# Kernel optimization log

Hardware: AMD Instinct MI355X
Metric: run time of the kernel (lower is better)

The kernel has to match this reference:

```python
import jax, jax.numpy as jnp
import numpy as np

GRID_SIZE = 8
MARGIN = 1.0
NUM_NEG = 4
SOS_NEG = 8
LOSS_LAMBDA = 1.0
IMG_H, IMG_W = 960, 1280  # desc2 is the stride-GRID_SIZE feature map of this image
BIG = 5.0    # fill for radius-masked entries in FOS distance matrix (> max unit-desc dist 2)
HUGE = 1e6   # fill for invalid entries in SOS candidate scores


def _l2n(x, eps=1e-8):
    return x / (jnp.linalg.norm(x, axis=-1, keepdims=True) + eps)


def _pdist(a, b, eps=1e-12):
    # a: B x N x C, b: B x M x C -> B x N x M euclidean distances
    sq = (jnp.sum(a * a, -1)[..., :, None] + jnp.sum(b * b, -1)[..., None, :]
          - 2.0 * jnp.einsum('bnc,bmc->bnm', a, b))
    return jnp.sqrt(jnp.maximum(sq, eps))


def _bilinear(desc, pts):
    # desc: B x C x H x W, pts: B x N x 2 in (y, x) image-pixel coords -> B x N x C
    B, C, H, W = desc.shape
    g = pts / GRID_SIZE - 0.5  # image coords -> feature-grid coords
    gy = jnp.clip(g[..., 0], 0.0, H - 1.0)
    gx = jnp.clip(g[..., 1], 0.0, W - 1.0)
    y0 = jnp.clip(jnp.floor(gy).astype(jnp.int32), 0, H - 2)
    x0 = jnp.clip(jnp.floor(gx).astype(jnp.int32), 0, W - 2)
    wy = (gy - y0)[:, None, :]
    wx = (gx - x0)[:, None, :]
    flat = desc.reshape(B, C, H * W)
    gat = lambda yi, xi: jnp.take_along_axis(flat, (yi * W + xi)[:, None, :], axis=2)
    v00, v01 = gat(y0, x0), gat(y0, x0 + 1)
    v10, v11 = gat(y0 + 1, x0), gat(y0 + 1, x0 + 1)
    out = (v00 * (1 - wy) * (1 - wx) + v01 * (1 - wy) * wx
           + v10 * wy * (1 - wx) + v11 * wy * wx)
    return out.transpose(0, 2, 1)


def _forward(kp1, w_kp1, kp1_desc, desc2, homo12):
    r = 2.0 * GRID_SIZE  # spatial masking radius
    d1 = _l2n(kp1_desc)                       # B x N x C
    w_desc = _l2n(_bilinear(desc2, w_kp1))    # B x N x C interpolated warped descriptors

    # visibility of kp1 under homography homo12 (kp stored as (y, x))
    ones = jnp.ones_like(kp1[..., :1])
    p = jnp.concatenate([kp1[..., 1:2], kp1[..., 0:1], ones], -1)  # (x, y, 1)
    q = jnp.einsum('bij,bnj->bni', homo12, p)
    qx = q[..., 0] / (q[..., 2] + 1e-8)
    qy = q[..., 1] / (q[..., 2] + 1e-8)
    vis = ((qx >= 0) & (qx < IMG_W) & (qy >= 0) & (qy < IMG_H)).astype(d1.dtype)
    denom = jnp.sum(vis) + 1e-8

    # ---- FOS: hard quad triplet with radius masking ----
    pos = jnp.sqrt(jnp.sum((d1 - w_desc) ** 2, -1) + 1e-12)  # B x N
    D = _pdist(d1, w_desc)          # B x N x N cross descriptor distances
    s22 = _pdist(w_kp1, w_kp1)      # B x N x N warped-coordinate distances
    Dm = jnp.where(s22 <= r, BIG, D)  # mask spatial near-positives (incl. diagonal)
    neg1 = -jax.lax.top_k(-Dm, NUM_NEG)[0]                       # hardest negs per row anchor
    neg2 = -jax.lax.top_k(-Dm.transpose(0, 2, 1), NUM_NEG)[0]    # per column anchor
    t1 = jnp.mean(jax.nn.relu(MARGIN + pos[..., None] - neg1), -1)
    t2 = jnp.mean(jax.nn.relu(MARGIN + pos[..., None] - neg2), -1)
    fos = jnp.sum(vis * 0.5 * (t1 + t2)) / denom

    # ---- SOS: radius-masked second-order similarity regularizer ----
    s11 = _pdist(kp1, kp1)
    d11 = _pdist(d1, d1)
    d22 = _pdist(w_desc, w_desc)
    valid = (s11 > r) & (s22 > r)
    score = jnp.where(valid, d11, HUGE)
    nscore, idx = jax.lax.top_k(-score, SOS_NEG)  # sos_neg hardest valid neighbors
    sel_d11 = -nscore
    sel_d22 = jnp.take_along_axis(d22, idx, axis=2)
    diff2 = jnp.where(sel_d11 < HUGE * 0.1, (sel_d11 - sel_d22) ** 2, 0.0)
    sos_i = jnp.sqrt(jnp.sum(diff2, -1) + 1e-12)
    sos = jnp.sum(vis * sos_i) / denom

    return (fos + sos) * LOSS_LAMBDA


def setup_inputs() -> dict:
    key = jax.random.key(0)
    k1, k2, k3, k4, k5 = jax.random.split(key, 5)
    B, N, C, H, W = 2, 4096, 128, 120, 160
    scale = jnp.array([IMG_H - 1.0, IMG_W - 1.0], dtype=jnp.float32)
    kp1 = jax.random.uniform(k1, (B, N, 2), dtype=jnp.float32) * scale
    w_kp1 = jax.random.uniform(k2, (B, N, 2), dtype=jnp.float32) * scale
    kp1_desc = jax.random.normal(k3, (B, N, C), dtype=jnp.float32)
    desc2 = jax.random.normal(k4, (B, C, H, W), dtype=jnp.float32)
    homo12 = (jnp.tile(jnp.eye(3, dtype=jnp.float32), (B, 1, 1))
              + 0.001 * jax.random.normal(k5, (B, 3, 3), dtype=jnp.float32))
    return {'kp1': kp1, 'w_kp1': w_kp1, 'kp1_desc': kp1_desc,
            'desc2': desc2, 'homo12': homo12}


def reference(kp1, w_kp1, kp1_desc, desc2, homo12):
    return _forward(kp1, w_kp1, kp1_desc, desc2, homo12)
```

## Files before the change

kernel.cpp:

```cpp
#include <hip/hip_runtime.h>
#include <hip/hip_fp16.h>
#include <math.h>

#define NPTS 4096
#define CDIM 128
#define FH 120
#define FW 160
#define PIX (FH * FW)

typedef __attribute__((ext_vector_type(8))) short short8_t;
typedef __attribute__((ext_vector_type(4))) float float4_t;
typedef __attribute__((ext_vector_type(2))) unsigned short ushort2_t;

#define OFF_FRAG  0
#define OFF_WDB   1048576
#define OFF_JA    1572864
#define OFF_JB    1605632
#define OFF_POS   1622016
#define OFF_VIS   1630208
#define OFF_ACC   1638400
#define OFF_D2T   2031632
#define OFF_PARTS 2031632
#define OFF_END   4489232

__device__ __forceinline__ unsigned short f2bf(float f) {
  unsigned int u = __float_as_uint(f);
  u = (u + 0x7fffu + ((u >> 16) & 1u)) >> 16;
  return (unsigned short)u;
}

__device__ __forceinline__ float wavesum(float v) {
#pragma unroll
  for (int off = 1; off < 64; off <<= 1) v += __shfl_xor(v, off, 64);
  return v;
}

typedef const __attribute__((address_space(1))) unsigned int gu32_t;
typedef __attribute__((address_space(3))) unsigned int lu32_t;
__device__ __forceinline__ void gl_lds16(const void* g, void* l) {
  __builtin_amdgcn_global_load_lds((gu32_t*)g, (lu32_t*)l, 16, 0, 0);
}

__global__ __launch_bounds__(256) void transpose_desc2(
    const float* __restrict__ d2, unsigned short* __restrict__ out) {
  __shared__ unsigned short tile[64][130];
  const int bp = blockIdx.x;
  const int b = bp / 300;
  const int p0 = (bp - b * 300) * 64;
  const int tid = threadIdx.x;
  const int grp = tid >> 6, lp = tid & 63;
#pragma unroll 4
  for (int r = 0; r < 32; ++r) {
    int c = (r << 2) | grp;
    float v = d2[((size_t)b * CDIM + c) * PIX + p0 + lp];
    tile[lp][c] = __half_as_ushort(__float2half(v));
  }
  __syncthreads();
  unsigned int* ob = (unsigned int*)(out + ((size_t)b * PIX + p0) * CDIM);
#pragma unroll
  for (int i = 0; i < 16; ++i) {
    int u = (i << 8) | tid;
    int p = u >> 6, cc = (u & 63) << 1;
    unsigned int lo = tile[p][cc], hi = tile[p][cc + 1];
    ob[u] = lo | (hi << 16);
  }
}

#define PREP_TAIL() do {                                                        \
  {                                                                             \
    const int T = (p & (NPTS - 1)) >> 4, cRow = p & 15;                         \
    const int kcL = lane >> 4, quadL = (lane >> 2) & 3, jjL = (lane & 3) * 2;   \
    const size_t off = (size_t)(quadL * 16 + cRow) * 8 + jjL;                   \
    const size_t tb = (((size_t)b * 256 + T) * 2) * 4;                          \
    ushort2_t st; st.x = f2bf(d0); st.y = f2bf(d1v);                            \
    ushort2_t sw; sw.x = f2bf(e0); sw.y = f2bf(e1);                             \
    *(ushort2_t*)(frag + (tb + kcL) * 512 + off) = st;                          \
    *(ushort2_t*)(frag + (tb + 4 + kcL) * 512 + off) = sw;                      \
    ushort2_t swr; swr.x = f2bf(e0); swr.y = f2bf(e1);                          \
    *(ushort2_t*)(wdb + (size_t)p * CDIM + c2) = swr;                           \
  }                                                                             \
  float dd0 = d0 - e0, dd1 = d1v - e1;                                          \
  float ssp = wavesum(dd0 * dd0 + dd1 * dd1);                                   \
  if (lane == 0) {                                                              \
    pos[p] = sqrtf(ssp + 1e-12f);                                               \
    float ky = kp1[p * 2 + 0], kx = kp1[p * 2 + 1];                             \
    jA[p] = make_float4(ky, kx, y, x);                                          \
    jB[p] = make_float2(n1, n2);                                                \
    const float* h = homo + b * 9;                                              \
    float t0 = h[0] * kx + h[1] * ky + h[2];                                    \
    float t1 = h[3] * kx + h[4] * ky + h[5];                                    \
    float t2 = h[6] * kx + h[7] * ky + h[8];                                    \
    float qx = t0 / (t2 + 1e-8f), qy = t1 / (t2 + 1e-8f);                       \
    vis[p] = (qx >= 0.0f && qx < 1280.0f && qy >= 0.0f && qy < 960.0f)          \
                 ? 1.0f : 0.0f;                                                 \
  }                                                                             \
} while (0)

__global__ __launch_bounds__(256) void prep_t(
    const float* __restrict__ kp1, const float* __restrict__ wkp1,
    const float* __restrict__ desc, const unsigned short* __restrict__ d2t,
    const float* __restrict__ homo,
    unsigned short* __restrict__ frag, unsigned short* __restrict__ wdb,
    float4* __restrict__ jA, float2* __restrict__ jB,
    float* __restrict__ pos, float* __restrict__ vis, float* __restrict__ acc) {
  const int tid = threadIdx.x;
  if (blockIdx.x == 0 && tid < 4) acc[tid] = 0.0f;
  const int p = blockIdx.x * 4 + (tid >> 6);
  const int lane = tid & 63;
  const int b = p >> 12;
  const int c2 = lane * 2;

  float2 v = *(const float2*)(desc + (size_t)p * CDIM + c2);
  float ss = wavesum(v.x * v.x + v.y * v.y);
  float inv = 1.0f / (sqrtf(ss) + 1e-8f);
  float d0 = v.x * inv, d1v = v.y * inv;
  float n1 = ss * inv * inv;

  float y = wkp1[p * 2 + 0], x = wkp1[p * 2 + 1];
  float gy = fminf(fmaxf(y * 0.125f - 0.5f, 0.0f), (float)(FH - 1));
  float gx = fminf(fmaxf(x * 0.125f - 0.5f, 0.0f), (float)(FW - 1));
  int y0 = (int)floorf(gy); y0 = min(max(y0, 0), FH - 2);
  int x0 = (int)floorf(gx); x0 = min(max(x0, 0), FW - 2);
  float wy = gy - (float)y0, wx = gx - (float)x0;
  float w00 = (1 - wy) * (1 - wx), w01 = (1 - wy) * wx;
  float w10 = wy * (1 - wx), w11 = wy * wx;
  const unsigned int* t00 = (const unsigned int*)
      (d2t + ((size_t)b * PIX + y0 * FW + x0) * CDIM) + lane;
  unsigned int u00 = t00[0], u01 = t00[64];
  unsigned int u10 = t00[FW * 64], u11 = t00[FW * 64 + 64];
  float2 f00 = __half22float2(*(const __half2*)&u00);
  float2 f01 = __half22float2(*(const __half2*)&u01);
  float2 f10 = __half22float2(*(const __half2*)&u10);
  float2 f11 = __half22float2(*(const __half2*)&u11);
  float wv0 = f00.x * w00 + f01.x * w01 + f10.x * w10 + f11.x * w11;
  float wv1 = f00.y * w00 + f01.y * w01 + f10.y * w10 + f11.y * w11;
  float ss2 = wavesum(wv0 * wv0 + wv1 * wv1);
  float inv2 = 1.0f / (sqrtf(ss2) + 1e-8f);
  float e0 = wv0 * inv2, e1 = wv1 * inv2;
  float n2 = ss2 * inv2 * inv2;

  PREP_TAIL();
}

__global__ __launch_bounds__(256) void prep_g(
    const float* __restrict__ kp1, const float* __restrict__ wkp1,
    const float* __restrict__ desc, const float* __restrict__ desc2,
    const float* __restrict__ homo,
    unsigned short* __restrict__ frag, unsigned short* __restrict__ wdb,
    float4* __restrict__ jA, float2* __restrict__ jB,
    float* __restrict__ pos, float* __restrict__ vis, float* __restrict__ acc) {
  const int tid = threadIdx.x;
  if (blockIdx.x == 0 && tid < 4) acc[tid] = 0.0f;
  const int p = blockIdx.x * 4 + (tid >> 6);
  const int lane = tid & 63;
  const int b = p >> 12;
  const int c2 = lane * 2;

  float2 v = *(const float2*)(desc + (size_t)p * CDIM + c2);
  float ss = wavesum(v.x * v.x + v.y * v.y);
  float inv = 1.0f / (sqrtf(ss) + 1e-8f);
  float d0 = v.x * inv, d1v = v.y * inv;
  float n1 = ss * inv * inv;

  float y = wkp1[p * 2 + 0], x = wkp1[p * 2 + 1];
  float gy = fminf(fmaxf(y * 0.125f - 0.5f, 0.0f), (float)(FH - 1));
  float gx = fminf(fmaxf(x * 0.125f - 0.5f, 0.0f), (float)(FW - 1));
  int y0 = (int)floorf(gy); y0 = min(max(y0, 0), FH - 2);
  int x0 = (int)floorf(gx); x0 = min(max(x0, 0), FW - 2);
  float wy = gy - (float)y0, wx = gx - (float)x0;
  float w00 = (1 - wy) * (1 - wx), w01 = (1 - wy) * wx;
  float w10 = wy * (1 - wx), w11 = wy * wx;
  const float* q0 = desc2 + ((size_t)b * CDIM + c2) * PIX + y0 * FW + x0;
  const float* q1 = q0 + PIX;
  float wv0 = q0[0] * w00 + q0[1] * w01 + q0[FW] * w10 + q0[FW + 1] * w11;
  float wv1 = q1[0] * w00 + q1[1] * w01 + q1[FW] * w10 + q1[FW + 1] * w11;
  float ss2 = wavesum(wv0 * wv0 + wv1 * wv1);
  float inv2 = 1.0f / (sqrtf(ss2) + 1e-8f);
  float e0 = wv0 * inv2, e1 = wv1 * inv2;
  float n2 = ss2 * inv2 * inv2;

  PREP_TAIL();
}

__device__ __forceinline__ void ins4m(float v, float* L) {
  float p0 = L[0]; L[0] = fmaxf(L[0], v);
  float p1 = L[1]; L[1] = __builtin_amdgcn_fmed3f(p0, L[1], v);
  float p2 = L[2]; L[2] = __builtin_amdgcn_fmed3f(p1, L[2], v);
  L[3] = __builtin_amdgcn_fmed3f(p2, L[3], v);
}
__device__ __forceinline__ void ins6m(float v, float* L) {
  float p0 = L[0]; L[0] = fmaxf(L[0], v);
  float p1 = L[1]; L[1] = __builtin_amdgcn_fmed3f(p0, L[1], v);
  float p2 = L[2]; L[2] = __builtin_amdgcn_fmed3f(p1, L[2], v);
  float p3 = L[3]; L[3] = __builtin_amdgcn_fmed3f(p2, L[3], v);
  float p4 = L[4]; L[4] = __builtin_amdgcn_fmed3f(p3, L[4], v);
  L[5] = __builtin_amdgcn_fmed3f(p4, L[5], v);
}
__device__ __forceinline__ void ins10m(float v, float* L) {
  float p0 = L[0]; L[0] = fmaxf(L[0], v);
  float pk = p0;
#pragma unroll
  for (int k = 1; k < 9; ++k) {
    float cur = L[k];
    L[k] = __builtin_amdgcn_fmed3f(pk, cur, v);
    pk = cur;
  }
  L[9] = __builtin_amdgcn_fmed3f(pk, L[9], v);
}

__device__ __forceinline__ float packkey(float s, int j) {
  return __uint_as_float((__float_as_uint(s) & 0xFFFFF000u) | (unsigned)j);
}

#define TILE_COMPUTE(AD, AW, NA, NB, J0) do {                                   \
  float4_t aD = {0,0,0,0}, aDt = {0,0,0,0}, a11 = {0,0,0,0};                    \
  _Pragma("unroll")                                                             \
  for (int kc = 0; kc < 4; ++kc) {                                              \
    aD  = __builtin_amdgcn_mfma_f32_16x16x32_bf16(AW[kc], Bd[kc], aD,  0,0,0);  \
    aDt = __builtin_amdgcn_mfma_f32_16x16x32_bf16(AD[kc], Bw[kc], aDt, 0,0,0);  \
    a11 = __builtin_amdgcn_mfma_f32_16x16x32_bf16(AD[kc], Bd[kc], a11, 0,0,0);  \
  }                                                                             \
  const float nj1[4] = {NA.x, NA.z, NB.x, NB.z};                                \
  const float nj2[4] = {NA.y, NA.w, NB.y, NB.w};                                \
  _Pragma("unroll")                                                             \
  for (int reg = 0; reg < 4; ++reg) {                                           \
    const int jj = (J0) + (quad << 2) + reg;                                    \
    ins4m(packkey(fmaf(2.0f, aD[reg],  -nj2[reg]), jj), fD);                    \
    ins4m(packkey(fmaf(2.0f, aDt[reg], -nj1[reg]), jj), fDt);                   \
    ins6m(packkey(fmaf(2.0f, a11[reg], -nj1[reg]), jj), fS);                    \
  }                                                                             \
} while (0)

__global__ __launch_bounds__(256, 4) void loss_main(
    const unsigned short* __restrict__ frag,
    const float2* __restrict__ jBg, float* __restrict__ parts) {
  __shared__ __align__(16) unsigned short bufA[2][4096];

  const int tid = threadIdx.x;
  const int bid = blockIdx.x;
  const int combo = ((bid & 7) << 1) | (bid >> 9);
  const int b   = combo >> 3;
  const int seg = combo & 7;
  const int g   = (bid >> 3) & 63;
  const int wave = tid >> 6, lane = tid & 63;
  const int quad = lane >> 4;
  const int base = b * NPTS;
  const int jbase = seg << 9;

  short8_t Bd[4], Bw[4];
  {
    const unsigned short* fb =
        frag + (((size_t)b * 256 + (g * 4 + wave)) * 8) * 512 + (size_t)lane * 8;
#pragma unroll
    for (int kc = 0; kc < 4; ++kc) {
      Bd[kc] = *(const short8_t*)(fb + kc * 512);
      Bw[kc] = *(const short8_t*)(fb + (4 + kc) * 512);
    }
  }

  float fD[4], fDt[4], fS[6];
#pragma unroll
  for (int k = 0; k < 4; ++k) { fD[k] = -1e30f; fDt[k] = -1e30f; }
#pragma unroll
  for (int k = 0; k < 6; ++k) fS[k] = -1e30f;

  const unsigned short* fa = frag + (((size_t)b * 256 + (jbase >> 4)) * 8) * 512;
  const float2* jbb = jBg + base;
  const int ch = wave << 1;

  gl_lds16(fa + (size_t)ch * 512 + lane * 8, &bufA[0][ch * 512]);
  gl_lds16(fa + (size_t)(ch + 1) * 512 + lane * 8, &bufA[0][(ch + 1) * 512]);
  __syncthreads();

  int cur = 0;
  for (int t = 0; t < 32; ++t) {
    if (t + 1 < 32) {
      const unsigned short* fn = fa + 4096;
      gl_lds16(fn + (size_t)ch * 512 + lane * 8, &bufA[cur ^ 1][ch * 512]);
      gl_lds16(fn + (size_t)(ch + 1) * 512 + lane * 8,
               &bufA[cur ^ 1][(ch + 1) * 512]);
    }
    const int j0 = jbase + (t << 4);
    float4 na = *(const float4*)(jbb + j0 + (quad << 2));
    float4 nb = *(const float4*)(jbb + j0 + (quad << 2) + 2);
    short8_t Ad[4], Aw[4];
#pragma unroll
    for (int kc = 0; kc < 4; ++kc) {
      Ad[kc] = *(const short8_t*)&bufA[cur][kc * 512 + (size_t)lane * 8];
      Aw[kc] = *(const short8_t*)&bufA[cur][(4 + kc) * 512 + (size_t)lane * 8];
    }
    TILE_COMPUTE(Ad, Aw, na, nb, j0);
    __syncthreads();
    cur ^= 1;
    fa += 4096;
  }

  float eD[6], eDt[6], eS[10];
#pragma unroll
  for (int k = 0; k < 4; ++k) { eD[k] = fD[k]; eDt[k] = fDt[k]; }
  eD[4] = eD[5] = eDt[4] = eDt[5] = -1e30f;
#pragma unroll
  for (int k = 0; k < 6; ++k) eS[k] = fS[k];
  eS[6] = eS[7] = eS[8] = eS[9] = -1e30f;

  {
    float tmp[10];
#pragma unroll
    for (int off = 16; off <= 32; off <<= 1) {
#pragma unroll
      for (int k = 0; k < 6; ++k) tmp[k] = eD[k];
#pragma unroll
      for (int k = 0; k < 6; ++k) ins6m(__shfl_xor(tmp[k], off, 64), eD);
#pragma unroll
      for (int k = 0; k < 6; ++k) tmp[k] = eDt[k];
#pragma unroll
      for (int k = 0; k < 6; ++k) ins6m(__shfl_xor(tmp[k], off, 64), eDt);
#pragma unroll
      for (int k = 0; k < 10; ++k) tmp[k] = eS[k];
#pragma unroll
      for (int k = 0; k < 10; ++k) ins10m(__shfl_xor(tmp[k], off, 64), eS);
    }
  }

  if (lane < 16) {
    float* P = parts + (size_t)(seg * 22) * 8192 +
               (base + g * 64 + wave * 16 + lane);
#pragma unroll
    for (int k = 0; k < 6; ++k) {
      P[(size_t)k * 8192] = eD[k];
      P[(size_t)(6 + k) * 8192] = eDt[k];
    }
#pragma unroll
    for (int k = 0; k < 10; ++k) P[(size_t)(12 + k) * 8192] = eS[k];
  }
}

__device__ __forceinline__ float bflo(unsigned int u) { return __uint_as_float(u << 16); }
__device__ __forceinline__ float bfhi(unsigned int u) { return __uint_as_float(u & 0xFFFF0000u); }

__global__ __launch_bounds__(256) void merge_filter(
    const float* __restrict__ parts, const float4* __restrict__ jAg,
    const float2* __restrict__ jBg, const float* __restrict__ posg,
    const float* __restrict__ visg, const unsigned short* __restrict__ wdb,
    float* __restrict__ accum, float* __restrict__ out) {
  __shared__ int sJ[256];
  __shared__ float sD11[256], sD22[256], sT[64], sVis[32], sN2[32];
  const int tid = threadIdx.x;
  const int a0 = blockIdx.x * 32;

  if (tid < 64) {
    const int al = tid & 31;
    const int type = tid >> 5;
    const int a = a0 + al;
    const int base = a & ~(NPTS - 1);
    float L[6];
#pragma unroll
    for (int k = 0; k < 6; ++k) L[k] = -1e30f;
    const float* P = parts + (size_t)(type * 6) * 8192 + a;
#pragma unroll
    for (int s = 0; s < 8; ++s) {
#pragma unroll
      for (int k = 0; k < 6; ++k) ins6m(P[(size_t)(s * 22 + k) * 8192], L);
    }
    const float4 own = jAg[a];
    const float2 nb = jBg[a];
    const float pv = posg[a];
    const float nsel = type ? nb.y : nb.x;
    float ts = 0.0f;
    int got = 0;
#pragma unroll
    for (int k = 0; k < 6; ++k) {
      int j = (int)(__float_as_uint(L[k]) & 0xFFFu);
      float4 jc = jAg[base + j];
      float dz = own.z - jc.z, dw = own.w - jc.w;
      if (got < 4 && dz * dz + dw * dw > 256.0f) {
        float d2 = nsel - L[k];
        ts += fmaxf(1.0f + pv - sqrtf(fmaxf(d2, 1e-12f)), 0.0f);
        got++;
      }
    }
    sT[tid] = ts;
  } else if (tid < 96) {
    const int al = tid - 64;
    const int a = a0 + al;
    const int base = a & ~(NPTS - 1);
    float S[10];
#pragma unroll
    for (int k = 0; k < 10; ++k) S[k] = -1e30f;
    const float* P = parts + (size_t)12 * 8192 + a;
#pragma unroll
    for (int s = 0; s < 8; ++s) {
#pragma unroll
      for (int k = 0; k < 10; ++k) ins10m(P[(size_t)(s * 22 + k) * 8192], S);
    }
    const float4 own = jAg[a];
    const float2 nb = jBg[a];
    int m = 0;
#pragma unroll
    for (int k = 0; k < 10; ++k) {
      int j = (int)(__float_as_uint(S[k]) & 0xFFFu);
      float4 jc = jAg[base + j];
      float ay = own.x - jc.x, ax = own.y - jc.y;
      float wz = own.z - jc.z, ww = own.w - jc.w;
      if (m < 8 && ay * ay + ax * ax > 256.0f && wz * wz + ww * ww > 256.0f) {
        sJ[al * 8 + m] = base + j;
        sD11[al * 8 + m] = sqrtf(fmaxf(nb.x - S[k], 1e-12f));
        m++;
      }
    }
    for (int k = m; k < 8; ++k) sJ[al * 8 + k] = -1;
    sVis[al] = visg[a];
    sN2[al] = nb.y;
  }
  __syncthreads();

  {
    const int slot = tid;
    const int al = slot >> 3;
    const int j = sJ[slot];
    float d22 = 0.0f;
    if (j >= 0) {
      const uint4* pi = (const uint4*)(wdb + (size_t)(a0 + al) * CDIM);
      const uint4* pj = (const uint4*)(wdb + (size_t)j * CDIM);
      float dot = 0.0f;
#pragma unroll
      for (int qq = 0; qq < 16; ++qq) {
        uint4 ui = pi[qq], uj = pj[qq];
        dot = fmaf(bflo(ui.x), bflo(uj.x), dot); dot = fmaf(bfhi(ui.x), bfhi(uj.x), dot);
        dot = fmaf(bflo(ui.y), bflo(uj.y), dot); dot = fmaf(bfhi(ui.y), bfhi(uj.y), dot);
        dot = fmaf(bflo(ui.z), bflo(uj.z), dot); dot = fmaf(bfhi(ui.z), bfhi(uj.z), dot);
        dot = fmaf(bflo(ui.w), bflo(uj.w), dot); dot = fmaf(bfhi(ui.w), bfhi(uj.w), dot);
      }
      d22 = sqrtf(fmaxf(sN2[al] + jBg[j].y - 2.0f * dot, 1e-12f));
    }
    sD22[slot] = d22;
  }
  __syncthreads();

  float contrib = 0.0f, vsum = 0.0f;
  if (tid < 32) {
    float s = 0.0f;
#pragma unroll
    for (int k = 0; k < 8; ++k) {
      if (sJ[tid * 8 + k] >= 0) {
        float d = sD11[tid * 8 + k] - sD22[tid * 8 + k];
        s = fmaf(d, d, s);
      }
    }
    contrib = sVis[tid] * (0.125f * (sT[tid] + sT[32 + tid]) + sqrtf(s + 1e-12f));
    vsum = sVis[tid];
  }
  if (tid < 64) {
#pragma unroll
    for (int off = 32; off >= 1; off >>= 1) {
      contrib += __shfl_down(contrib, off, 64);
      vsum += __shfl_down(vsum, off, 64);
    }
    if (tid == 0) {
      atomicAdd(&accum[0], contrib);
      atomicAdd(&accum[1], vsum);
      __threadfence();
      float old = atomicAdd(&accum[2], 1.0f);
      if (old == 255.0f) {
        float t = atomicAdd(&accum[0], 0.0f);
        float v = atomicAdd(&accum[1], 0.0f);
        out[0] = t / (v + 1e-8f);
      }
    }
  }
}

extern "C" void kernel_launch(void* const* d_in, const int* in_sizes, int n_in,
                              void* d_out, int out_size, void* d_ws, size_t ws_size,
                              hipStream_t stream) {
  (void)in_sizes; (void)n_in; (void)out_size;
  const float* kp1   = (const float*)d_in[0];
  const float* wkp1  = (const float*)d_in[1];
  const float* desc  = (const float*)d_in[2];
  const float* desc2 = (const float*)d_in[3];
  const float* homo  = (const float*)d_in[4];
  float* ws = (float*)d_ws;
  unsigned short* frag = (unsigned short*)(ws + OFF_FRAG);
  unsigned short* wdb  = (unsigned short*)(ws + OFF_WDB);
  float4* jA = (float4*)(ws + OFF_JA);
  float2* jB = (float2*)(ws + OFF_JB);
  float* pos = ws + OFF_POS;
  float* vis = ws + OFF_VIS;
  float* acc = ws + OFF_ACC;
  float* parts = ws + OFF_PARTS;
  unsigned short* d2t = (unsigned short*)(ws + OFF_D2T);

  if (ws_size >= (size_t)OFF_END * 4) {
    transpose_desc2<<<600, 256, 0, stream>>>(desc2, d2t);
    prep_t<<<2048, 256, 0, stream>>>(kp1, wkp1, desc, d2t, homo,
                                     frag, wdb, jA, jB, pos, vis, acc);
  } else {
    prep_g<<<2048, 256, 0, stream>>>(kp1, wkp1, desc, desc2, homo,
                                     frag, wdb, jA, jB, pos, vis, acc);
  }
  loss_main<<<1024, 256, 0, stream>>>(frag, jB, parts);
  merge_filter<<<256, 256, 0, stream>>>(parts, jA, jB, pos, vis, wdb, acc,
                                        (float*)d_out);
}
```

Baseline: 152.2 us.

## Pre-scale norms into MFMA accumulator init and stage two tiles per barrier

Per-point squared norms are stored pre-scaled as -0.5*n in separate arrays and used to initialise the MFMA accumulators. This removes the per-element fmaf and the norm-shuffle code in the inner scoring loop, and the downstream distance formulas are rescaled to match. The loss_main loop now loads two 16-row fragment tiles per LDS stage with double buffering, halving the number of __syncthreads per tile at the cost of twice the LDS. Keys now hold half the original score, which slightly changes how precision truncation in packkey affects ordering.

```diff
diff --git a/kernel.cpp b/kernel.cpp
--- a/kernel.cpp
+++ b/kernel.cpp
@@ -85,7 +85,8 @@
     pos[p] = sqrtf(ssp + 1e-12f);                                               \
     float ky = kp1[p * 2 + 0], kx = kp1[p * 2 + 1];                             \
     jA[p] = make_float4(ky, kx, y, x);                                          \
-    jB[p] = make_float2(n1, n2);                                                \
+    jb1[p] = -0.5f * n1;                                                        \
+    jb2[p] = -0.5f * n2;                                                        \
     const float* h = homo + b * 9;                                              \
     float t0 = h[0] * kx + h[1] * ky + h[2];                                    \
     float t1 = h[3] * kx + h[4] * ky + h[5];                                    \
@@ -101,7 +102,7 @@
     const float* __restrict__ desc, const unsigned short* __restrict__ d2t,
     const float* __restrict__ homo,
     unsigned short* __restrict__ frag, unsigned short* __restrict__ wdb,
-    float4* __restrict__ jA, float2* __restrict__ jB,
+    float4* __restrict__ jA, float* __restrict__ jb1, float* __restrict__ jb2,
     float* __restrict__ pos, float* __restrict__ vis, float* __restrict__ acc) {
   const int tid = threadIdx.x;
   if (blockIdx.x == 0 && tid < 4) acc[tid] = 0.0f;
@@ -147,7 +148,7 @@
     const float* __restrict__ desc, const float* __restrict__ desc2,
     const float* __restrict__ homo,
     unsigned short* __restrict__ frag, unsigned short* __restrict__ wdb,
-    float4* __restrict__ jA, float2* __restrict__ jB,
+    float4* __restrict__ jA, float* __restrict__ jb1, float* __restrict__ jb2,
     float* __restrict__ pos, float* __restrict__ vis, float* __restrict__ acc) {
   const int tid = threadIdx.x;
   if (blockIdx.x == 0 && tid < 4) acc[tid] = 0.0f;
@@ -212,29 +213,46 @@
   return __uint_as_float((__float_as_uint(s) & 0xFFFFF000u) | (unsigned)j);
 }
 
-#define TILE_COMPUTE(AD, AW, NA, NB, J0) do {                                   \
-  float4_t aD = {0,0,0,0}, aDt = {0,0,0,0}, a11 = {0,0,0,0};                    \
+#define TILE_ONE(BUF, J0) do {                                                  \
+  const float4 m1 = *(const float4*)(j1b + (J0) + (quad << 2));                 \
+  const float4 m2 = *(const float4*)(j2b + (J0) + (quad << 2));                 \
+  short8_t Ad[4], Aw[4];                                                        \
   _Pragma("unroll")                                                             \
   for (int kc = 0; kc < 4; ++kc) {                                              \
-    aD  = __builtin_amdgcn_mfma_f32_16x16x32_bf16(AW[kc], Bd[kc], aD,  0,0,0);  \
-    aDt = __builtin_amdgcn_mfma_f32_16x16x32_bf16(AD[kc], Bw[kc], aDt, 0,0,0);  \
-    a11 = __builtin_amdgcn_mfma_f32_16x16x32_bf16(AD[kc], Bd[kc], a11, 0,0,0);  \
+    Ad[kc] = *(const short8_t*)&(BUF)[kc * 512 + lane * 8];                     \
+    Aw[kc] = *(const short8_t*)&(BUF)[(4 + kc) * 512 + lane * 8];               \
   }                                                                             \
-  const float nj1[4] = {NA.x, NA.z, NB.x, NB.z};                                \
-  const float nj2[4] = {NA.y, NA.w, NB.y, NB.w};                                \
+  float4_t aD, aDt, a11;                                                        \
+  aD[0] = m2.x; aD[1] = m2.y; aD[2] = m2.z; aD[3] = m2.w;                       \
+  aDt[0] = m1.x; aDt[1] = m1.y; aDt[2] = m1.z; aDt[3] = m1.w;                   \
+  a11 = aDt;                                                                    \
+  _Pragma("unroll")                                                             \
+  for (int kc = 0; kc < 4; ++kc) {                                              \
+    aD  = __builtin_amdgcn_mfma_f32_16x16x32_bf16(Aw[kc], Bd[kc], aD,  0,0,0);  \
+    aDt = __builtin_amdgcn_mfma_f32_16x16x32_bf16(Ad[kc], Bw[kc], aDt, 0,0,0);  \
+    a11 = __builtin_amdgcn_mfma_f32_16x16x32_bf16(Ad[kc], Bd[kc], a11, 0,0,0);  \
+  }                                                                             \
   _Pragma("unroll")                                                             \
   for (int reg = 0; reg < 4; ++reg) {                                           \
     const int jj = (J0) + (quad << 2) + reg;                                    \
-    ins4m(packkey(fmaf(2.0f, aD[reg],  -nj2[reg]), jj), fD);                    \
-    ins4m(packkey(fmaf(2.0f, aDt[reg], -nj1[reg]), jj), fDt);                   \
-    ins6m(packkey(fmaf(2.0f, a11[reg], -nj1[reg]), jj), fS);                    \
+    ins4m(packkey(aD[reg], jj), fD);                                            \
+    ins4m(packkey(aDt[reg], jj), fDt);                                          \
+    ins6m(packkey(a11[reg], jj), fS);                                           \
   }                                                                             \
 } while (0)
 
+#define STAGE2(DST, TGLOB) do {                                                  \
+  gl_lds16((TGLOB) + ch * 512 + lane * 8, &DST[0][ch * 512]);                    \
+  gl_lds16((TGLOB) + (ch + 1) * 512 + lane * 8, &DST[0][(ch + 1) * 512]);        \
+  gl_lds16((TGLOB) + 4096 + ch * 512 + lane * 8, &DST[1][ch * 512]);             \
+  gl_lds16((TGLOB) + 4096 + (ch + 1) * 512 + lane * 8, &DST[1][(ch + 1) * 512]); \
+} while (0)
+
 __global__ __launch_bounds__(256, 4) void loss_main(
     const unsigned short* __restrict__ frag,
-    const float2* __restrict__ jBg, float* __restrict__ parts) {
-  __shared__ __align__(16) unsigned short bufA[2][4096];
+    const float* __restrict__ jb1g, const float* __restrict__ jb2g,
+    float* __restrict__ parts) {
+  __shared__ __align__(16) unsigned short buf[2][2][4096];
 
   const int tid = threadIdx.x;
   const int bid = blockIdx.x;
@@ -265,34 +283,23 @@
   for (int k = 0; k < 6; ++k) fS[k] = -1e30f;
 
   const unsigned short* fa = frag + (((size_t)b * 256 + (jbase >> 4)) * 8) * 512;
-  const float2* jbb = jBg + base;
+  const float* j1b = jb1g + base;
+  const float* j2b = jb2g + base;
   const int ch = wave << 1;
 
-  gl_lds16(fa + (size_t)ch * 512 + lane * 8, &bufA[0][ch * 512]);
-  gl_lds16(fa + (size_t)(ch + 1) * 512 + lane * 8, &bufA[0][(ch + 1) * 512]);
+  STAGE2(buf[0], fa);
   __syncthreads();
 
-  int cur = 0;
-  for (int t = 0; t < 32; ++t) {
-    if (t + 1 < 32) {
-      const unsigned short* fn = fa + 4096;
-      gl_lds16(fn + (size_t)ch * 512 + lane * 8, &bufA[cur ^ 1][ch * 512]);
-      gl_lds16(fn + (size_t)(ch + 1) * 512 + lane * 8,
-               &bufA[cur ^ 1][(ch + 1) * 512]);
-    }
-    const int j0 = jbase + (t << 4);
-    float4 na = *(const float4*)(jbb + j0 + (quad << 2));
-    float4 nb = *(const float4*)(jbb + j0 + (quad << 2) + 2);
-    short8_t Ad[4], Aw[4];
-#pragma unroll
-    for (int kc = 0; kc < 4; ++kc) {
-      Ad[kc] = *(const short8_t*)&bufA[cur][kc * 512 + (size_t)lane * 8];
-      Aw[kc] = *(const short8_t*)&bufA[cur][(4 + kc) * 512 + (size_t)lane * 8];
-    }
-    TILE_COMPUTE(Ad, Aw, na, nb, j0);
+  for (int t = 0; t < 32; t += 4) {
+    STAGE2(buf[1], fa + 8192);
+    TILE_ONE(buf[0][0], jbase + (t << 4));
+    TILE_ONE(buf[0][1], jbase + ((t + 1) << 4));
     __syncthreads();
-    cur ^= 1;
-    fa += 4096;
+    if (t + 4 < 32) STAGE2(buf[0], fa + 16384);
+    TILE_ONE(buf[1][0], jbase + ((t + 2) << 4));
+    TILE_ONE(buf[1][1], jbase + ((t + 3) << 4));
+    __syncthreads();
+    fa += 16384;
   }
 
   float eD[6], eDt[6], eS[10];
@@ -340,7 +347,8 @@
 
 __global__ __launch_bounds__(256) void merge_filter(
     const float* __restrict__ parts, const float4* __restrict__ jAg,
-    const float2* __restrict__ jBg, const float* __restrict__ posg,
+    const float* __restrict__ jb1g, const float* __restrict__ jb2g,
+    const float* __restrict__ posg,
     const float* __restrict__ visg, const unsigned short* __restrict__ wdb,
     float* __restrict__ accum, float* __restrict__ out) {
   __shared__ int sJ[256];
@@ -363,9 +371,8 @@
       for (int k = 0; k < 6; ++k) ins6m(P[(size_t)(s * 22 + k) * 8192], L);
     }
     const float4 own = jAg[a];
-    const float2 nb = jBg[a];
     const float pv = posg[a];
-    const float nsel = type ? nb.y : nb.x;
+    const float nsel = -2.0f * (type ? jb2g[a] : jb1g[a]);
     float ts = 0.0f;
     int got = 0;
 #pragma unroll
@@ -374,7 +381,7 @@
       float4 jc = jAg[base + j];
       float dz = own.z - jc.z, dw = own.w - jc.w;
       if (got < 4 && dz * dz + dw * dw > 256.0f) {
-        float d2 = nsel - L[k];
+        float d2 = fmaf(-2.0f, L[k], nsel);
         ts += fmaxf(1.0f + pv - sqrtf(fmaxf(d2, 1e-12f)), 0.0f);
         got++;
       }
@@ -394,7 +401,7 @@
       for (int k = 0; k < 10; ++k) ins10m(P[(size_t)(s * 22 + k) * 8192], S);
     }
     const float4 own = jAg[a];
-    const float2 nb = jBg[a];
+    const float n1i = -2.0f * jb1g[a];
     int m = 0;
 #pragma unroll
     for (int k = 0; k < 10; ++k) {
@@ -404,13 +411,13 @@
       float wz = own.z - jc.z, ww = own.w - jc.w;
       if (m < 8 && ay * ay + ax * ax > 256.0f && wz * wz + ww * ww > 256.0f) {
         sJ[al * 8 + m] = base + j;
-        sD11[al * 8 + m] = sqrtf(fmaxf(nb.x - S[k], 1e-12f));
+        sD11[al * 8 + m] = sqrtf(fmaxf(fmaf(-2.0f, S[k], n1i), 1e-12f));
         m++;
       }
     }
     for (int k = m; k < 8; ++k) sJ[al * 8 + k] = -1;
     sVis[al] = visg[a];
-    sN2[al] = nb.y;
+    sN2[al] = -2.0f * jb2g[a];
   }
   __syncthreads();
 
@@ -431,7 +438,7 @@
         dot = fmaf(bflo(ui.z), bflo(uj.z), dot); dot = fmaf(bfhi(ui.z), bfhi(uj.z), dot);
         dot = fmaf(bflo(ui.w), bflo(uj.w), dot); dot = fmaf(bfhi(ui.w), bfhi(uj.w), dot);
       }
-      d22 = sqrtf(fmaxf(sN2[al] + jBg[j].y - 2.0f * dot, 1e-12f));
+      d22 = sqrtf(fmaxf(fmaf(-2.0f, jb2g[j] + dot, sN2[al]), 1e-12f));
     }
     sD22[slot] = d22;
   }
@@ -483,7 +490,8 @@
   unsigned short* frag = (unsigned short*)(ws + OFF_FRAG);
   unsigned short* wdb  = (unsigned short*)(ws + OFF_WDB);
   float4* jA = (float4*)(ws + OFF_JA);
-  float2* jB = (float2*)(ws + OFF_JB);
+  float* jb1 = ws + OFF_JB;
+  float* jb2 = ws + OFF_JB + 8192;
   float* pos = ws + OFF_POS;
   float* vis = ws + OFF_VIS;
   float* acc = ws + OFF_ACC;
@@ -493,12 +501,12 @@
   if (ws_size >= (size_t)OFF_END * 4) {
     transpose_desc2<<<600, 256, 0, stream>>>(desc2, d2t);
     prep_t<<<2048, 256, 0, stream>>>(kp1, wkp1, desc, d2t, homo,
-                                     frag, wdb, jA, jB, pos, vis, acc);
+                                     frag, wdb, jA, jb1, jb2, pos, vis, acc);
   } else {
     prep_g<<<2048, 256, 0, stream>>>(kp1, wkp1, desc, desc2, homo,
-                                     frag, wdb, jA, jB, pos, vis, acc);
-  }
-  loss_main<<<1024, 256, 0, stream>>>(frag, jB, parts);
-  merge_filter<<<256, 256, 0, stream>>>(parts, jA, jB, pos, vis, wdb, acc,
+                                     frag, wdb, jA, jb1, jb2, pos, vis, acc);
+  }
+  loss_main<<<1024, 256, 0, stream>>>(frag, jb1, jb2, parts);
+  merge_filter<<<256, 256, 0, stream>>>(parts, jA, jb1, jb2, pos, vis, wdb, acc,
                                         (float*)d_out);
 }
```

New measurement: 148.5 us, median of 2. 2.4% less time.
